# Optimization experiments

Measured on AMD Instinct MI355X. Metric: run time of the kernel, lower is better.

## Reference

```python
import jax, jax.numpy as jnp
import numpy as np

B, S, H = 4, 1024, 1024
NH, HD = 16, 64          # heads, head_dim (NH*HD == H)
E, K, I = 8, 2, 1024     # routed experts, top_k, expert intermediate
NSH = 2                  # shared experts -> shared intermediate = NSH*I
EPS = 1e-6


def setup_inputs() -> dict:
    key = jax.random.key(0)
    ks = jax.random.split(key, 12)
    init = lambda k, shape: (jax.random.normal(k, shape, jnp.float32) * 0.02)
    return {
        "hidden_states": jax.random.normal(ks[0], (B, S, H), jnp.float32),
        "conditioning": jax.random.normal(ks[1], (B, H), jnp.float32),
        "adaLN_W": init(ks[2], (H, 6 * H)),
        "ln1_scale": jnp.ones((H,), jnp.float32),
        "ln1_bias": jnp.zeros((H,), jnp.float32),
        "ln2_scale": jnp.ones((H,), jnp.float32),
        "ln2_bias": jnp.zeros((H,), jnp.float32),
        "Wq": init(ks[3], (H, H)),
        "Wk": init(ks[4], (H, H)),
        "Wv": init(ks[5], (H, H)),
        "Wo": init(ks[6], (H, H)),
        "gate_kernel": init(ks[7], (E, H)),
        "We1": init(ks[8], (E, H, I)),
        "We2": init(ks[9], (E, I, H)),
        "Ws1": init(ks[10], (H, NSH * I)),
        "Ws2": init(ks[11], (NSH * I, H)),
    }


def _layernorm(x, scale, bias):
    m = x.mean(-1, keepdims=True)
    v = x.var(-1, keepdims=True)
    return (x - m) * jax.lax.rsqrt(v + EPS) * scale + bias


def _modulate(x, shift, scale):
    # (1 + scale) * x + shift, broadcasting [B,H] conditioning over seq dim
    return x * (1.0 + scale[:, None, :]) + shift[:, None, :]


def _attention(x, Wq, Wk, Wv, Wo):
    b, s, h = x.shape
    q = (x @ Wq).reshape(b, s, NH, HD)
    k = (x @ Wk).reshape(b, s, NH, HD)
    v = (x @ Wv).reshape(b, s, NH, HD)
    scores = jnp.einsum("bqnd,bknd->bnqk", q, k) / np.sqrt(HD).astype(np.float32)
    probs = jax.nn.softmax(scores, axis=-1)
    out = jnp.einsum("bnqk,bknd->bqnd", probs, v).reshape(b, s, h)
    return out @ Wo


def reference(hidden_states, conditioning, adaLN_W, ln1_scale, ln1_bias,
              ln2_scale, ln2_bias, Wq, Wk, Wv, Wo, gate_kernel, We1, We2,
              Ws1, Ws2):
    # adaLN modulation: SiLU -> Linear(H, 6H) -> chunk 6
    mods = jax.nn.silu(conditioning) @ adaLN_W  # [B, 6H]
    (shift_msa, scale_msa, gate_msa,
     shift_mlp, scale_mlp, gate_mlp) = jnp.split(mods, 6, axis=-1)

    normed = _modulate(_layernorm(hidden_states, ln1_scale, ln1_bias),
                       shift_msa, scale_msa)
    attn_out = _attention(normed, Wq, Wk, Wv, Wo)
    h = hidden_states + gate_msa[:, None, :] * attn_out

    normed2 = _modulate(_layernorm(h, ln2_scale, ln2_bias),
                        shift_mlp, scale_mlp)

    # --- MoE gate (DeepSeek-V2 style, greedy top-k, softmax scoring) ---
    logits = jnp.einsum("bsh,eh->bse", normed2.astype(jnp.float32),
                        gate_kernel.astype(jnp.float32))
    scores = jax.nn.softmax(logits, axis=-1)           # [B,S,E]
    topk_w, topk_idx = jax.lax.top_k(scores, K)        # [B,S,K]
    topk_w = topk_w / (topk_w.sum(-1, keepdims=True) + 1e-20)  # norm_topk_prob

    # --- dense all-expert MLPs then top-k combine (as in DiTMLPMoE) ---
    eh = jax.nn.gelu(jnp.einsum("bsh,ehi->ebsi", normed2, We1))  # [E,B,S,I]
    eo = jnp.einsum("ebsi,eih->bseh", eh, We2)                   # [B,S,E,H]
    sel = jnp.take_along_axis(eo, topk_idx[..., None], axis=2)   # [B,S,K,H]
    y = (sel * topk_w[..., None].astype(sel.dtype)).sum(axis=2)  # [B,S,H]

    # shared experts (always active)
    y = y + jax.nn.gelu(normed2 @ Ws1) @ Ws2

    return h + gate_mlp[:, None, :] * y
```

## Files before the change

### kernel.cpp

```cpp
#include <hip/hip_runtime.h>

typedef __bf16 bf16x8 __attribute__((ext_vector_type(8)));
typedef __bf16 bf16x4 __attribute__((ext_vector_type(4)));
typedef float  f32x4  __attribute__((ext_vector_type(4)));

__device__ inline float wred_sum(float v){
  #pragma unroll
  for (int d = 1; d < 64; d <<= 1) v += __shfl_xor(v, d, 64);
  return v;
}

__device__ inline float gelu_t(float x){
  const float c0 = 0.7978845608028654f;
  float t = tanhf(c0 * (x + 0.044715f * x * x * x));
  return 0.5f * x * (1.0f + t);
}

__device__ __forceinline__ void gload_lds16(const __bf16* g, __bf16* l){
  __builtin_amdgcn_global_load_lds((const __attribute__((address_space(1))) void*)g,
                                   (__attribute__((address_space(3))) void*)l, 16, 0, 0);
}

__global__ __launch_bounds__(256)
void transpose_cvt(const float* __restrict__ in, __bf16* __restrict__ out, int R, int C){
  long mo = (long)blockIdx.z * R * C;
  in += mo; out += mo;
  __shared__ float t[32][33];
  int r0 = blockIdx.y * 32, c0 = blockIdx.x * 32;
  int tid = threadIdx.x;
  int tr = tid >> 3, tc = (tid & 7) * 4;
  float4 vv = *(const float4*)&in[(long)(r0 + tr) * C + c0 + tc];
  t[tr][tc + 0] = vv.x; t[tr][tc + 1] = vv.y; t[tr][tc + 2] = vv.z; t[tr][tc + 3] = vv.w;
  __syncthreads();
  int oc = tid >> 3, orr = (tid & 7) * 4;
  bf16x4 o4;
  #pragma unroll
  for (int i = 0; i < 4; i++) o4[i] = (__bf16)t[orr + i][oc];
  *(bf16x4*)&out[(long)(c0 + oc) * R + r0 + orr] = o4;
}

__global__ __launch_bounds__(256)
void adaln_k(const float* __restrict__ cond, const float* __restrict__ W, float* __restrict__ mods){
  int b = blockIdx.y, z = blockIdx.z;
  int col = (blockIdx.x * 256 + threadIdx.x) * 4;
  __shared__ float sc[256];
  int h2 = z * 256 + threadIdx.x;
  float x = cond[b * 1024 + h2];
  sc[threadIdx.x] = x / (1.f + expf(-x));
  __syncthreads();
  float a0 = 0.f, a1 = 0.f, a2 = 0.f, a3 = 0.f;
  #pragma unroll 4
  for (int i = 0; i < 256; i++){
    float s = sc[i];
    float4 wv = *(const float4*)&W[(long)(z * 256 + i) * 6144 + col];
    a0 += s * wv.x; a1 += s * wv.y; a2 += s * wv.z; a3 += s * wv.w;
  }
  atomicAdd(&mods[b * 6144 + col + 0], a0);
  atomicAdd(&mods[b * 6144 + col + 1], a1);
  atomicAdd(&mods[b * 6144 + col + 2], a2);
  atomicAdd(&mods[b * 6144 + col + 3], a3);
}

__global__ __launch_bounds__(256)
void ln_mod(const float* __restrict__ x, const float* __restrict__ sc, const float* __restrict__ bi,
            const float* __restrict__ mods, int shift_off, int scale_off, __bf16* __restrict__ out){
  int row = blockIdx.x, tid = threadIdx.x, b = row >> 10;
  float4 xv = *(const float4*)&x[(long)row * 1024 + tid * 4];
  float s  = xv.x + xv.y + xv.z + xv.w;
  float s2 = xv.x * xv.x + xv.y * xv.y + xv.z * xv.z + xv.w * xv.w;
  s = wred_sum(s); s2 = wred_sum(s2);
  __shared__ float ssum[4], ssum2[4];
  int w = tid >> 6;
  if ((tid & 63) == 0){ ssum[w] = s; ssum2[w] = s2; }
  __syncthreads();
  s = ssum[0] + ssum[1] + ssum[2] + ssum[3];
  s2 = ssum2[0] + ssum2[1] + ssum2[2] + ssum2[3];
  float mean = s * (1.f / 1024.f);
  float var  = s2 * (1.f / 1024.f) - mean * mean;
  float inv  = rsqrtf(var + 1e-6f);
  const float xa[4] = {xv.x, xv.y, xv.z, xv.w};
  #pragma unroll
  for (int i = 0; i < 4; i++){
    int c = tid * 4 + i;
    float nv = (xa[i] - mean) * inv * sc[c] + bi[c];
    nv = nv * (1.f + mods[b * 6144 + scale_off + c]) + mods[b * 6144 + shift_off + c];
    out[(long)row * 1024 + c] = (__bf16)nv;
  }
}

__global__ __launch_bounds__(256)
void gate_k(const float* __restrict__ h, const float* __restrict__ ln2s, const float* __restrict__ ln2b,
            const float* __restrict__ mods, const float* __restrict__ gw,
            int* __restrict__ eidx, float* __restrict__ wpair){
  __shared__ float gws[8192];
  int tid = threadIdx.x;
  #pragma unroll
  for (int i = 0; i < 8; i++){
    int idx = tid + i * 256;
    *(float4*)&gws[idx * 4] = *(const float4*)&gw[idx * 4];
  }
  __syncthreads();
  int wv = tid >> 6, lane = tid & 63;
  int tok = blockIdx.x * 4 + wv;
  int b = tok >> 10;
  float4 xv[4]; float s = 0.f, s2 = 0.f;
  #pragma unroll
  for (int ch = 0; ch < 4; ch++){
    float4 v = *(const float4*)&h[(long)tok * 1024 + ch * 256 + lane * 4];
    xv[ch] = v;
    s  += v.x + v.y + v.z + v.w;
    s2 += v.x * v.x + v.y * v.y + v.z * v.z + v.w * v.w;
  }
  s = wred_sum(s); s2 = wred_sum(s2);
  float mean = s * (1.f / 1024.f);
  float var  = s2 * (1.f / 1024.f) - mean * mean;
  float inv  = rsqrtf(var + 1e-6f);
  float lg[8];
  #pragma unroll
  for (int e = 0; e < 8; e++) lg[e] = 0.f;
  #pragma unroll
  for (int ch = 0; ch < 4; ch++){
    int c = ch * 256 + lane * 4;
    float4 s4  = *(const float4*)&ln2s[c];
    float4 b4  = *(const float4*)&ln2b[c];
    float4 sc4 = *(const float4*)&mods[b * 6144 + 4096 + c];
    float4 sh4 = *(const float4*)&mods[b * 6144 + 3072 + c];
    float n0 = ((xv[ch].x - mean) * inv * s4.x + b4.x) * (1.f + sc4.x) + sh4.x;
    float n1 = ((xv[ch].y - mean) * inv * s4.y + b4.y) * (1.f + sc4.y) + sh4.y;
    float n2 = ((xv[ch].z - mean) * inv * s4.z + b4.z) * (1.f + sc4.z) + sh4.z;
    float n3 = ((xv[ch].w - mean) * inv * s4.w + b4.w) * (1.f + sc4.w) + sh4.w;
    #pragma unroll
    for (int e = 0; e < 8; e++){
      float4 g4 = *(const float4*)&gws[e * 1024 + c];
      lg[e] += n0 * g4.x + n1 * g4.y + n2 * g4.z + n3 * g4.w;
    }
  }
  #pragma unroll
  for (int e = 0; e < 8; e++) lg[e] = wred_sum(lg[e]);
  if (lane == 0){
    float mx = lg[0];
    #pragma unroll
    for (int e = 1; e < 8; e++) mx = fmaxf(mx, lg[e]);
    float p[8], ss = 0.f;
    #pragma unroll
    for (int e = 0; e < 8; e++){ p[e] = expf(lg[e] - mx); ss += p[e]; }
    #pragma unroll
    for (int e = 0; e < 8; e++) p[e] /= ss;
    int i0 = 0; float b0 = p[0];
    #pragma unroll
    for (int e = 1; e < 8; e++) if (p[e] > b0){ b0 = p[e]; i0 = e; }
    int i1 = -1; float b1 = -1.f;
    #pragma unroll
    for (int e = 0; e < 8; e++) if (e != i0 && p[e] > b1){ b1 = p[e]; i1 = e; }
    float dn = b0 + b1 + 1e-20f;
    eidx[tok * 2]     = i0; wpair[tok * 2]     = b0 / dn;
    eidx[tok * 2 + 1] = i1; wpair[tok * 2 + 1] = b1 / dn;
  }
}

__global__ __launch_bounds__(256)
void build_k(const int* __restrict__ eidx, int* __restrict__ counts, int* __restrict__ lists){
  int e = blockIdx.x;
  int tid = threadIdx.x, wv = tid >> 6, lane = tid & 63;
  __shared__ int base;
  __shared__ int woff[4];
  if (tid == 0) base = 0;
  __syncthreads();
  for (int it = 0; it < 32; ++it){
    int i = it * 256 + tid;
    bool m = (eidx[i] == e);
    unsigned long long bal = __ballot(m);
    int prefix = __popcll(bal & ((1ull << lane) - 1ull));
    if (lane == 0) woff[wv] = __popcll(bal);
    __syncthreads();
    int off = base;
    #pragma unroll
    for (int k = 0; k < 4; k++) if (k < wv) off += woff[k];
    if (m) lists[e * 4096 + off + prefix] = i;
    __syncthreads();
    if (tid == 0) base += woff[0] + woff[1] + woff[2] + woff[3];
    __syncthreads();
  }
  if (tid == 0) counts[e] = base;
}

__global__ __launch_bounds__(256)
void attn_k(const __bf16* __restrict__ qkv, __bf16* __restrict__ og){
  int bh = blockIdx.y; int bb = bh >> 4, hn = bh & 15;
  int q0 = blockIdx.x * 128;
  long tokbase = (long)bb * 1024;
  int hd0 = hn * 64;
  int tid = threadIdx.x; int w = tid >> 6; int lane = tid & 63;

  __shared__ __bf16 Ks[64][76];
  __shared__ __bf16 Vt[64][76];
  __shared__ __bf16 Ps[4][32][76];

  const float QS = 0.125f * 1.44269504088896f;
  bf16x8 qf[2][2];
  #pragma unroll
  for (int sub = 0; sub < 2; sub++){
    long qrow = tokbase + q0 + sub * 64 + w * 16 + (lane & 15);
    qf[sub][0] = *(const bf16x8*)&qkv[qrow * 3072 + hd0 + (lane >> 4) * 8];
    qf[sub][1] = *(const bf16x8*)&qkv[qrow * 3072 + hd0 + 32 + (lane >> 4) * 8];
    #pragma unroll
    for (int i = 0; i < 8; i++){
      qf[sub][0][i] = (__bf16)((float)qf[sub][0][i] * QS);
      qf[sub][1][i] = (__bf16)((float)qf[sub][1][i] * QS);
    }
  }

  __bf16 one_b = (__bf16)1.0f;
  bf16x8 one8 = (bf16x8){one_b, one_b, one_b, one_b, one_b, one_b, one_b, one_b};

  float m_r[2][4];
  f32x4 oa[2][4];
  f32x4 lacc[2];
  #pragma unroll
  for (int sub = 0; sub < 2; sub++){
    lacc[sub] = (f32x4){0.f, 0.f, 0.f, 0.f};
    #pragma unroll
    for (int r = 0; r < 4; r++) m_r[sub][r] = -1e30f;
    #pragma unroll
    for (int hb = 0; hb < 4; hb++) oa[sub][hb] = (f32x4){0.f, 0.f, 0.f, 0.f};
  }

  int dcol = tid & 63, rblk = tid >> 6;
  for (int t = 0; t < 16; t++){
    long kvbase = tokbase + t * 64;
    #pragma unroll
    for (int p = 0; p < 2; p++){
      int r = (tid >> 3) + p * 32;
      int c = (tid & 7) * 8;
      *(bf16x8*)&Ks[r][c] = *(const bf16x8*)&qkv[(kvbase + r) * 3072 + 1024 + hd0 + c];
    }
    bf16x8 col0, col1;
    #pragma unroll
    for (int i = 0; i < 8; i++)
      col0[i] = qkv[(kvbase + rblk * 16 + i) * 3072 + 2048 + hd0 + dcol];
    #pragma unroll
    for (int i = 0; i < 8; i++)
      col1[i] = qkv[(kvbase + rblk * 16 + 8 + i) * 3072 + 2048 + hd0 + dcol];
    *(bf16x8*)&Vt[dcol][rblk * 16]     = col0;
    *(bf16x8*)&Vt[dcol][rblk * 16 + 8] = col1;
    __syncthreads();

    #pragma unroll
    for (int sub = 0; sub < 2; sub++){
      f32x4 sf[4];
      #pragma unroll
      for (int cb = 0; cb < 4; cb++){
        bf16x8 kf0 = *(const bf16x8*)&Ks[cb * 16 + (lane & 15)][(lane >> 4) * 8];
        bf16x8 kf1 = *(const bf16x8*)&Ks[cb * 16 + (lane & 15)][32 + (lane >> 4) * 8];
        f32x4 sacc = (f32x4){0.f, 0.f, 0.f, 0.f};
        sacc = __builtin_amdgcn_mfma_f32_16x16x32_bf16(qf[sub][0], kf0, sacc, 0, 0, 0);
        sacc = __builtin_amdgcn_mfma_f32_16x16x32_bf16(qf[sub][1], kf1, sacc, 0, 0, 0);
        sf[cb] = sacc;
      }
      float mxr[4]; float dmax = -1e30f;
      #pragma unroll
      for (int r = 0; r < 4; r++){
        float mx = fmaxf(fmaxf(sf[0][r], sf[1][r]), fmaxf(sf[2][r], sf[3][r]));
        #pragma unroll
        for (int d = 1; d < 16; d <<= 1) mx = fmaxf(mx, __shfl_xor(mx, d, 64));
        mxr[r] = mx;
        dmax = fmaxf(dmax, mx - m_r[sub][r]);
      }
      if (!__all(dmax <= 8.f)){
        #pragma unroll
        for (int r = 0; r < 4; r++){
          float mn = fmaxf(m_r[sub][r], mxr[r]);
          float fr = __builtin_amdgcn_exp2f(m_r[sub][r] - mn);
          m_r[sub][r] = mn;
          lacc[sub][r] *= fr;
          #pragma unroll
          for (int hb = 0; hb < 4; hb++) oa[sub][hb][r] *= fr;
        }
      }
      #pragma unroll
      for (int cb = 0; cb < 4; cb++)
        #pragma unroll
        for (int r = 0; r < 4; r++)
          Ps[w][sub * 16 + (lane >> 4) * 4 + r][cb * 16 + (lane & 15)] =
            (__bf16)__builtin_amdgcn_exp2f(sf[cb][r] - m_r[sub][r]);
    }
    bf16x8 pf[2][2];
    #pragma unroll
    for (int sub = 0; sub < 2; sub++){
      pf[sub][0] = *(const bf16x8*)&Ps[w][sub * 16 + (lane & 15)][(lane >> 4) * 8];
      pf[sub][1] = *(const bf16x8*)&Ps[w][sub * 16 + (lane & 15)][32 + (lane >> 4) * 8];
      lacc[sub] = __builtin_amdgcn_mfma_f32_16x16x32_bf16(pf[sub][0], one8, lacc[sub], 0, 0, 0);
      lacc[sub] = __builtin_amdgcn_mfma_f32_16x16x32_bf16(pf[sub][1], one8, lacc[sub], 0, 0, 0);
    }
    #pragma unroll
    for (int hb = 0; hb < 4; hb++){
      bf16x8 vf0 = *(const bf16x8*)&Vt[hb * 16 + (lane & 15)][(lane >> 4) * 8];
      bf16x8 vf1 = *(const bf16x8*)&Vt[hb * 16 + (lane & 15)][32 + (lane >> 4) * 8];
      #pragma unroll
      for (int sub = 0; sub < 2; sub++){
        oa[sub][hb] = __builtin_amdgcn_mfma_f32_16x16x32_bf16(pf[sub][0], vf0, oa[sub][hb], 0, 0, 0);
        oa[sub][hb] = __builtin_amdgcn_mfma_f32_16x16x32_bf16(pf[sub][1], vf1, oa[sub][hb], 0, 0, 0);
      }
    }
    __syncthreads();
  }
  #pragma unroll
  for (int sub = 0; sub < 2; sub++)
    #pragma unroll
    for (int hb = 0; hb < 4; hb++)
      #pragma unroll
      for (int r = 0; r < 4; r++){
        long row = tokbase + q0 + sub * 64 + w * 16 + (lane >> 4) * 4 + r;
        float val = oa[sub][hb][r] / lacc[sub][r];
        og[row * 1024 + hd0 + hb * 16 + (lane & 15)] = (__bf16)val;
      }
}

template<int EPI, int GMODE>
__global__ __launch_bounds__(256)
void gemm_k(const __bf16* __restrict__ A, int lda,
            const __bf16* __restrict__ Bt, int K, long bstride,
            const int* __restrict__ lists, const int* __restrict__ counts,
            __bf16* __restrict__ outb, int ldo,
            float* __restrict__ outf,
            const float* __restrict__ resid,
            const float* __restrict__ mods, int mod_off,
            const float* __restrict__ wpair){
  int e = blockIdx.z;
  int cnt = 1 << 30;
  const int* list = nullptr;
  if (GMODE){
    cnt = counts[e];
    if ((int)blockIdx.y * 128 >= cnt) return;
    list = lists + e * 4096;
    Bt += (long)e * bstride;
  }
  int row0 = blockIdx.y * 128;
  int n0 = blockIdx.x * 128;
  int tid = threadIdx.x;
  int lane = tid & 63, w = tid >> 6;
  int wr = (w >> 1) * 64, wc = (w & 1) * 64;

  __shared__ __bf16 As[128 * 64];
  __shared__ __bf16 Bs[128 * 64];

  f32x4 acc[4][4];
  #pragma unroll
  for (int m = 0; m < 4; m++)
    #pragma unroll
    for (int n = 0; n < 4; n++) acc[m][n] = (f32x4){0.f, 0.f, 0.f, 0.f};

  long aoff[4]; const __bf16* bptr[4];
  #pragma unroll
  for (int j = 0; j < 4; j++){
    int r = w * 32 + j * 8 + (lane >> 3);
    int scb = (lane & 7) ^ (r & 7);
    int gr = row0 + r;
    int srcr;
    if (GMODE == 0) srcr = gr;
    else if (gr < cnt){ int pv = list[gr]; srcr = (GMODE == 1) ? (pv >> 1) : pv; }
    else { int pv = list[0]; srcr = (GMODE == 1) ? (pv >> 1) : pv; }
    aoff[j] = (long)srcr * lda + scb * 8;
    bptr[j] = Bt + (long)(n0 + r) * K + scb * 8;
  }
  const int nk = K / 64;
  for (int kt = 0; kt < nk; ++kt){
    int k0 = kt * 64;
    #pragma unroll
    for (int j = 0; j < 4; j++){
      gload_lds16(A + aoff[j] + k0, &As[(w * 32 + j * 8) * 64]);
      gload_lds16(bptr[j] + k0,     &Bs[(w * 32 + j * 8) * 64]);
    }
    __syncthreads();
    #pragma unroll
    for (int ks = 0; ks < 2; ++ks){
      bf16x8 af[4], bfr[4];
      #pragma unroll
      for (int m = 0; m < 4; m++){
        int r = wr + m * 16 + (lane & 15);
        int blk = (ks * 4 + (lane >> 4)) ^ (r & 7);
        af[m] = *(const bf16x8*)&As[r * 64 + blk * 8];
      }
      #pragma unroll
      for (int n = 0; n < 4; n++){
        int r = wc + n * 16 + (lane & 15);
        int blk = (ks * 4 + (lane >> 4)) ^ (r & 7);
        bfr[n] = *(const bf16x8*)&Bs[r * 64 + blk * 8];
      }
      #pragma unroll
      for (int m = 0; m < 4; m++)
        #pragma unroll
        for (int n = 0; n < 4; n++)
          acc[m][n] = __builtin_amdgcn_mfma_f32_16x16x32_bf16(af[m], bfr[n], acc[m][n], 0, 0, 0);
    }
    __syncthreads();
  }
  #pragma unroll
  for (int m = 0; m < 4; m++){
    #pragma unroll
    for (int r = 0; r < 4; r++){
      int rl = wr + m * 16 + (lane >> 4) * 4 + r;
      int grow = row0 + rl;
      if (GMODE && grow >= cnt) continue;
      #pragma unroll
      for (int n = 0; n < 4; n++){
        int col = n0 + wc + n * 16 + (lane & 15);
        float v = acc[m][n][r];
        if (EPI == 0){
          outb[(long)grow * ldo + col] = (__bf16)v;
        } else if (EPI == 1){
          int dst = (GMODE == 1) ? list[grow] : grow;
          outb[(long)dst * ldo + col] = (__bf16)gelu_t(v);
        } else if (EPI == 2){
          int b = grow >> 10;
          outf[(long)grow * 1024 + col] = resid[(long)grow * 1024 + col] + mods[b * 6144 + mod_off + col] * v;
        } else if (EPI == 3){
          outf[(long)grow * 1024 + col] = v;
        } else if (EPI == 4){
          int pv = list[grow];
          atomicAdd(&outf[(long)(pv >> 1) * 1024 + col], wpair[pv] * v);
        }
      }
    }
  }
}

__global__ __launch_bounds__(256)
void final_k(const float* __restrict__ h, const float* __restrict__ y,
             const float* __restrict__ mods, float* __restrict__ out){
  int i = blockIdx.x * 256 + threadIdx.x;
  long base = (long)i * 4;
  int row = (int)(base >> 10); int b = row >> 10; int c = (int)(base & 1023);
  float4 hv = *(const float4*)&h[base];
  float4 yv = *(const float4*)&y[base];
  const float* g = &mods[b * 6144 + 5120 + c];
  float4 o;
  o.x = hv.x + g[0] * yv.x;
  o.y = hv.y + g[1] * yv.y;
  o.z = hv.z + g[2] * yv.z;
  o.w = hv.w + g[3] * yv.w;
  *(float4*)&out[base] = o;
}

extern "C" void kernel_launch(void* const* d_in, const int* in_sizes, int n_in,
                              void* d_out, int out_size, void* d_ws, size_t ws_size,
                              hipStream_t stream){
  const float* hidden = (const float*)d_in[0];
  const float* cond   = (const float*)d_in[1];
  const float* adaW   = (const float*)d_in[2];
  const float* ln1s   = (const float*)d_in[3];
  const float* ln1b   = (const float*)d_in[4];
  const float* ln2s   = (const float*)d_in[5];
  const float* ln2b   = (const float*)d_in[6];
  const float* Wq     = (const float*)d_in[7];
  const float* Wk     = (const float*)d_in[8];
  const float* Wv     = (const float*)d_in[9];
  const float* Wo     = (const float*)d_in[10];
  const float* gatek  = (const float*)d_in[11];
  const float* We1    = (const float*)d_in[12];
  const float* We2    = (const float*)d_in[13];
  const float* Ws1    = (const float*)d_in[14];
  const float* Ws2    = (const float*)d_in[15];
  float* out = (float*)d_out;

  const size_t MB = 1024 * 1024;
  char* W = (char*)d_ws;
  size_t off = 0;
  auto take = [&](size_t b) -> void* {
    void* p = W + off;
    off += (b + 255) & ~((size_t)255);
    return p;
  };
  float*  mods   = (float*) take(4 * 6144 * sizeof(float));
  __bf16* qkvT   = (__bf16*)take(6 * MB);
  __bf16* WoT    = (__bf16*)take(2 * MB);
  __bf16* Ws1T   = (__bf16*)take(4 * MB);
  __bf16* Ws2T   = (__bf16*)take(4 * MB);
  __bf16* We1T   = (__bf16*)take(16 * MB);
  __bf16* We2T   = (__bf16*)take(16 * MB);
  __bf16* n1     = (__bf16*)take(8 * MB);
  __bf16* ab     = (__bf16*)take(8 * MB);
  __bf16* qkv    = (__bf16*)take(24 * MB);
  float*  hb     = (float*) take(16 * MB);
  __bf16* n2     = (__bf16*)take(8 * MB);
  float*  yb     = (float*) take(16 * MB);
  int*    counts = (int*)   take(256);
  int*    lists  = (int*)   take(8 * 4096 * 4);
  float*  wpair  = (float*) take(8192 * 4);
  int*    eidx   = (int*)   take(8192 * 4);
  __bf16* EH = n1;
  __bf16* SH = qkv;

  dim3 blk(256);

  hipMemsetAsync(mods, 0, 4 * 6144 * sizeof(float), stream);

  transpose_cvt<<<dim3(32, 32, 1), blk, 0, stream>>>(Wq,  qkvT,              1024, 1024);
  transpose_cvt<<<dim3(32, 32, 1), blk, 0, stream>>>(Wk,  qkvT + 1024*1024,  1024, 1024);
  transpose_cvt<<<dim3(32, 32, 1), blk, 0, stream>>>(Wv,  qkvT + 2048*1024,  1024, 1024);
  transpose_cvt<<<dim3(32, 32, 1), blk, 0, stream>>>(Wo,  WoT,  1024, 1024);
  transpose_cvt<<<dim3(64, 32, 1), blk, 0, stream>>>(Ws1, Ws1T, 1024, 2048);
  transpose_cvt<<<dim3(32, 64, 1), blk, 0, stream>>>(Ws2, Ws2T, 2048, 1024);
  transpose_cvt<<<dim3(32, 32, 8), blk, 0, stream>>>(We1, We1T, 1024, 1024);
  transpose_cvt<<<dim3(32, 32, 8), blk, 0, stream>>>(We2, We2T, 1024, 1024);

  adaln_k<<<dim3(6, 4, 4), blk, 0, stream>>>(cond, adaW, mods);

  ln_mod<<<4096, blk, 0, stream>>>(hidden, ln1s, ln1b, mods, 0, 1024, n1);

  gemm_k<0, 0><<<dim3(24, 32, 1), blk, 0, stream>>>(n1, 1024, qkvT, 1024, 0, nullptr, nullptr, qkv, 3072, nullptr, nullptr, nullptr, 0, nullptr);

  attn_k<<<dim3(8, 64, 1), blk, 0, stream>>>(qkv, ab);

  gemm_k<2, 0><<<dim3(8, 32, 1), blk, 0, stream>>>(ab, 1024, WoT, 1024, 0, nullptr, nullptr, nullptr, 0, hb, hidden, mods, 2048, nullptr);

  ln_mod<<<4096, blk, 0, stream>>>(hb, ln2s, ln2b, mods, 3072, 4096, n2);

  gate_k<<<1024, blk, 0, stream>>>(hb, ln2s, ln2b, mods, gatek, eidx, wpair);
  build_k<<<8, blk, 0, stream>>>(eidx, counts, lists);

  gemm_k<1, 0><<<dim3(16, 32, 1), blk, 0, stream>>>(n2, 1024, Ws1T, 1024, 0, nullptr, nullptr, SH, 2048, nullptr, nullptr, nullptr, 0, nullptr);
  gemm_k<3, 0><<<dim3(8, 32, 1), blk, 0, stream>>>(SH, 2048, Ws2T, 2048, 0, nullptr, nullptr, nullptr, 0, yb, nullptr, nullptr, 0, nullptr);

  gemm_k<1, 1><<<dim3(8, 32, 8), blk, 0, stream>>>(n2, 1024, We1T, 1024, 1048576, lists, counts, EH, 1024, nullptr, nullptr, nullptr, 0, nullptr);
  gemm_k<4, 2><<<dim3(8, 32, 8), blk, 0, stream>>>(EH, 1024, We2T, 1024, 1048576, lists, counts, nullptr, 0, yb, nullptr, nullptr, 0, wpair);

  final_k<<<4096, blk, 0, stream>>>(hb, yb, mods, out);

  (void)in_sizes; (void)n_in; (void)out_size; (void)ws_size;
}
```

Baseline: 561.7 us.

## Fuse transposes, LN2 into gate, final combine into shared GEMM; double-buffer GEMM LDS

All weight transposes now run in one launch. adaLN is restructured so each block handles all four batches and reuses each weight load. The second layernorm-modulate is folded into the gate kernel, and the final residual/gate combine is folded into the shared-expert down-projection epilogue, which removes two launches and a full activation pass. The routed-expert accumulator is zeroed by the same memset. The GEMM main loop gains double-buffered LDS with prefetch of the next K tile, doubling shared memory use and possibly lowering occupancy. Attention blocks are also remapped so neighbouring blocks share KV.

New measurement: 560.9 us. About the same (-0.1%).

```diff
diff --git a/kernel.cpp b/kernel.cpp
--- a/kernel.cpp
+++ b/kernel.cpp
@@ -22,43 +22,58 @@
 }
 
 __global__ __launch_bounds__(256)
-void transpose_cvt(const float* __restrict__ in, __bf16* __restrict__ out, int R, int C){
-  long mo = (long)blockIdx.z * R * C;
-  in += mo; out += mo;
+void transpose_all(const float* __restrict__ Wq, const float* __restrict__ Wk,
+                   const float* __restrict__ Wv, const float* __restrict__ Wo,
+                   const float* __restrict__ Ws1, const float* __restrict__ Ws2,
+                   const float* __restrict__ We1, const float* __restrict__ We2,
+                   __bf16* __restrict__ qkvT, __bf16* __restrict__ WoT,
+                   __bf16* __restrict__ Ws1T, __bf16* __restrict__ Ws2T,
+                   __bf16* __restrict__ We1T, __bf16* __restrict__ We2T){
+  int z = blockIdx.z;
+  const float* src; long ss; __bf16* dst; long ds;
+  const long M1 = 1024 * 1024;
+  if (z < 3)      { src = (z == 0 ? Wq : z == 1 ? Wk : Wv); ss = 1024; dst = qkvT + (long)z * M1; ds = 1024; }
+  else if (z == 3){ src = Wo; ss = 1024; dst = WoT; ds = 1024; }
+  else if (z < 6) { int ch = z - 4; src = Ws1 + ch * 1024; ss = 2048; dst = Ws1T + (long)ch * M1; ds = 1024; }
+  else if (z < 8) { int rh = z - 6; src = Ws2 + (long)rh * M1; ss = 1024; dst = Ws2T + rh * 1024; ds = 2048; }
+  else if (z < 16){ int e = z - 8;  src = We1 + (long)e * M1; ss = 1024; dst = We1T + (long)e * M1; ds = 1024; }
+  else            { int e = z - 16; src = We2 + (long)e * M1; ss = 1024; dst = We2T + (long)e * M1; ds = 1024; }
   __shared__ float t[32][33];
   int r0 = blockIdx.y * 32, c0 = blockIdx.x * 32;
   int tid = threadIdx.x;
   int tr = tid >> 3, tc = (tid & 7) * 4;
-  float4 vv = *(const float4*)&in[(long)(r0 + tr) * C + c0 + tc];
+  float4 vv = *(const float4*)&src[(long)(r0 + tr) * ss + c0 + tc];
   t[tr][tc + 0] = vv.x; t[tr][tc + 1] = vv.y; t[tr][tc + 2] = vv.z; t[tr][tc + 3] = vv.w;
   __syncthreads();
   int oc = tid >> 3, orr = (tid & 7) * 4;
   bf16x4 o4;
   #pragma unroll
   for (int i = 0; i < 4; i++) o4[i] = (__bf16)t[orr + i][oc];
-  *(bf16x4*)&out[(long)(c0 + oc) * R + r0 + orr] = o4;
+  *(bf16x4*)&dst[(long)(c0 + oc) * ds + r0 + orr] = o4;
 }
 
 __global__ __launch_bounds__(256)
 void adaln_k(const float* __restrict__ cond, const float* __restrict__ W, float* __restrict__ mods){
-  int b = blockIdx.y, z = blockIdx.z;
-  int col = (blockIdx.x * 256 + threadIdx.x) * 4;
-  __shared__ float sc[256];
-  int h2 = z * 256 + threadIdx.x;
-  float x = cond[b * 1024 + h2];
-  sc[threadIdx.x] = x / (1.f + expf(-x));
+  int col = blockIdx.x * 256 + threadIdx.x;
+  int kc  = blockIdx.y;
+  __shared__ float sc[4][256];
+  for (int i = threadIdx.x; i < 1024; i += 256){
+    int b = i >> 8, r = i & 255;
+    float x = cond[b * 1024 + kc * 256 + r];
+    sc[b][r] = x / (1.f + expf(-x));
+  }
   __syncthreads();
   float a0 = 0.f, a1 = 0.f, a2 = 0.f, a3 = 0.f;
   #pragma unroll 4
   for (int i = 0; i < 256; i++){
-    float s = sc[i];
-    float4 wv = *(const float4*)&W[(long)(z * 256 + i) * 6144 + col];
-    a0 += s * wv.x; a1 += s * wv.y; a2 += s * wv.z; a3 += s * wv.w;
-  }
-  atomicAdd(&mods[b * 6144 + col + 0], a0);
-  atomicAdd(&mods[b * 6144 + col + 1], a1);
-  atomicAdd(&mods[b * 6144 + col + 2], a2);
-  atomicAdd(&mods[b * 6144 + col + 3], a3);
+    float wv = W[(long)(kc * 256 + i) * 6144 + col];
+    a0 += sc[0][i] * wv; a1 += sc[1][i] * wv;
+    a2 += sc[2][i] * wv; a3 += sc[3][i] * wv;
+  }
+  atomicAdd(&mods[0 * 6144 + col], a0);
+  atomicAdd(&mods[1 * 6144 + col], a1);
+  atomicAdd(&mods[2 * 6144 + col], a2);
+  atomicAdd(&mods[3 * 6144 + col], a3);
 }
 
 __global__ __launch_bounds__(256)
@@ -91,7 +106,7 @@
 __global__ __launch_bounds__(256)
 void gate_k(const float* __restrict__ h, const float* __restrict__ ln2s, const float* __restrict__ ln2b,
             const float* __restrict__ mods, const float* __restrict__ gw,
-            int* __restrict__ eidx, float* __restrict__ wpair){
+            int* __restrict__ eidx, float* __restrict__ wpair, __bf16* __restrict__ n2o){
   __shared__ float gws[8192];
   int tid = threadIdx.x;
   #pragma unroll
@@ -125,14 +140,15 @@
     float4 b4  = *(const float4*)&ln2b[c];
     float4 sc4 = *(const float4*)&mods[b * 6144 + 4096 + c];
     float4 sh4 = *(const float4*)&mods[b * 6144 + 3072 + c];
-    float n0 = ((xv[ch].x - mean) * inv * s4.x + b4.x) * (1.f + sc4.x) + sh4.x;
-    float n1 = ((xv[ch].y - mean) * inv * s4.y + b4.y) * (1.f + sc4.y) + sh4.y;
-    float n2 = ((xv[ch].z - mean) * inv * s4.z + b4.z) * (1.f + sc4.z) + sh4.z;
-    float n3 = ((xv[ch].w - mean) * inv * s4.w + b4.w) * (1.f + sc4.w) + sh4.w;
+    float v0 = ((xv[ch].x - mean) * inv * s4.x + b4.x) * (1.f + sc4.x) + sh4.x;
+    float v1 = ((xv[ch].y - mean) * inv * s4.y + b4.y) * (1.f + sc4.y) + sh4.y;
+    float v2 = ((xv[ch].z - mean) * inv * s4.z + b4.z) * (1.f + sc4.z) + sh4.z;
+    float v3 = ((xv[ch].w - mean) * inv * s4.w + b4.w) * (1.f + sc4.w) + sh4.w;
+    *(bf16x4*)&n2o[(long)tok * 1024 + c] = (bf16x4){(__bf16)v0, (__bf16)v1, (__bf16)v2, (__bf16)v3};
     #pragma unroll
     for (int e = 0; e < 8; e++){
       float4 g4 = *(const float4*)&gws[e * 1024 + c];
-      lg[e] += n0 * g4.x + n1 * g4.y + n2 * g4.z + n3 * g4.w;
+      lg[e] += v0 * g4.x + v1 * g4.y + v2 * g4.z + v3 * g4.w;
     }
   }
   #pragma unroll
@@ -186,8 +202,11 @@
 
 __global__ __launch_bounds__(256)
 void attn_k(const __bf16* __restrict__ qkv, __bf16* __restrict__ og){
-  int bh = blockIdx.y; int bb = bh >> 4, hn = bh & 15;
-  int q0 = blockIdx.x * 128;
+  int p = blockIdx.x + blockIdx.y * 8;
+  int qblk = (p >> 3) & 7;
+  int bh   = (p & 7) + ((p >> 6) << 3);
+  int bb = bh >> 4, hn = bh & 15;
+  int q0 = qblk * 128;
   long tokbase = (long)bb * 1024;
   int hd0 = hn * 64;
   int tid = threadIdx.x; int w = tid >> 6; int lane = tid & 63;
@@ -229,8 +248,8 @@
   for (int t = 0; t < 16; t++){
     long kvbase = tokbase + t * 64;
     #pragma unroll
-    for (int p = 0; p < 2; p++){
-      int r = (tid >> 3) + p * 32;
+    for (int pp = 0; pp < 2; pp++){
+      int r = (tid >> 3) + pp * 32;
       int c = (tid & 7) * 8;
       *(bf16x8*)&Ks[r][c] = *(const bf16x8*)&qkv[(kvbase + r) * 3072 + 1024 + hd0 + c];
     }
@@ -325,7 +344,8 @@
             float* __restrict__ outf,
             const float* __restrict__ resid,
             const float* __restrict__ mods, int mod_off,
-            const float* __restrict__ wpair){
+            const float* __restrict__ wpair,
+            const float* __restrict__ addin){
   int e = blockIdx.z;
   int cnt = 1 << 30;
   const int* list = nullptr;
@@ -341,8 +361,8 @@
   int lane = tid & 63, w = tid >> 6;
   int wr = (w >> 1) * 64, wc = (w & 1) * 64;
 
-  __shared__ __bf16 As[128 * 64];
-  __shared__ __bf16 Bs[128 * 64];
+  __shared__ __bf16 As[2 * 128 * 64];
+  __shared__ __bf16 Bs[2 * 128 * 64];
 
   f32x4 acc[4][4];
   #pragma unroll
@@ -364,14 +384,23 @@
     bptr[j] = Bt + (long)(n0 + r) * K + scb * 8;
   }
   const int nk = K / 64;
+  #pragma unroll
+  for (int j = 0; j < 4; j++){
+    gload_lds16(A + aoff[j], &As[(w * 32 + j * 8) * 64]);
+    gload_lds16(bptr[j],     &Bs[(w * 32 + j * 8) * 64]);
+  }
+  __syncthreads();
+  int cur = 0;
   for (int kt = 0; kt < nk; ++kt){
-    int k0 = kt * 64;
-    #pragma unroll
-    for (int j = 0; j < 4; j++){
-      gload_lds16(A + aoff[j] + k0, &As[(w * 32 + j * 8) * 64]);
-      gload_lds16(bptr[j] + k0,     &Bs[(w * 32 + j * 8) * 64]);
-    }
-    __syncthreads();
+    int nxt = cur ^ 1;
+    if (kt + 1 < nk){
+      int k0 = (kt + 1) * 64;
+      #pragma unroll
+      for (int j = 0; j < 4; j++){
+        gload_lds16(A + aoff[j] + k0, &As[nxt * 8192 + (w * 32 + j * 8) * 64]);
+        gload_lds16(bptr[j] + k0,     &Bs[nxt * 8192 + (w * 32 + j * 8) * 64]);
+      }
+    }
     #pragma unroll
     for (int ks = 0; ks < 2; ++ks){
       bf16x8 af[4], bfr[4];
@@ -379,13 +408,13 @@
       for (int m = 0; m < 4; m++){
         int r = wr + m * 16 + (lane & 15);
         int blk = (ks * 4 + (lane >> 4)) ^ (r & 7);
-        af[m] = *(const bf16x8*)&As[r * 64 + blk * 8];
+        af[m] = *(const bf16x8*)&As[cur * 8192 + r * 64 + blk * 8];
       }
       #pragma unroll
       for (int n = 0; n < 4; n++){
         int r = wc + n * 16 + (lane & 15);
         int blk = (ks * 4 + (lane >> 4)) ^ (r & 7);
-        bfr[n] = *(const bf16x8*)&Bs[r * 64 + blk * 8];
+        bfr[n] = *(const bf16x8*)&Bs[cur * 8192 + r * 64 + blk * 8];
       }
       #pragma unroll
       for (int m = 0; m < 4; m++)
@@ -394,6 +423,7 @@
           acc[m][n] = __builtin_amdgcn_mfma_f32_16x16x32_bf16(af[m], bfr[n], acc[m][n], 0, 0, 0);
     }
     __syncthreads();
+    cur = nxt;
   }
   #pragma unroll
   for (int m = 0; m < 4; m++){
@@ -414,32 +444,17 @@
         } else if (EPI == 2){
           int b = grow >> 10;
           outf[(long)grow * 1024 + col] = resid[(long)grow * 1024 + col] + mods[b * 6144 + mod_off + col] * v;
-        } else if (EPI == 3){
-          outf[(long)grow * 1024 + col] = v;
         } else if (EPI == 4){
           int pv = list[grow];
           atomicAdd(&outf[(long)(pv >> 1) * 1024 + col], wpair[pv] * v);
+        } else if (EPI == 5){
+          int b = grow >> 10;
+          outf[(long)grow * 1024 + col] = resid[(long)grow * 1024 + col]
+              + mods[b * 6144 + mod_off + col] * (v + addin[(long)grow * 1024 + col]);
         }
       }
     }
   }
-}
-
-__global__ __launch_bounds__(256)
-void final_k(const float* __restrict__ h, const float* __restrict__ y,
-             const float* __restrict__ mods, float* __restrict__ out){
-  int i = blockIdx.x * 256 + threadIdx.x;
-  long base = (long)i * 4;
-  int row = (int)(base >> 10); int b = row >> 10; int c = (int)(base & 1023);
-  float4 hv = *(const float4*)&h[base];
-  float4 yv = *(const float4*)&y[base];
-  const float* g = &mods[b * 6144 + 5120 + c];
-  float4 o;
-  o.x = hv.x + g[0] * yv.x;
-  o.y = hv.y + g[1] * yv.y;
-  o.z = hv.z + g[2] * yv.z;
-  o.w = hv.w + g[3] * yv.w;
-  *(float4*)&out[base] = o;
 }
 
 extern "C" void kernel_launch(void* const* d_in, const int* in_sizes, int n_in,
@@ -472,6 +487,7 @@
     return p;
   };
   float*  mods   = (float*) take(4 * 6144 * sizeof(float));
+  float*  yb     = (float*) take(16 * MB);
   __bf16* qkvT   = (__bf16*)take(6 * MB);
   __bf16* WoT    = (__bf16*)take(2 * MB);
   __bf16* Ws1T   = (__bf16*)take(4 * MB);
@@ -483,7 +499,6 @@
   __bf16* qkv    = (__bf16*)take(24 * MB);
   float*  hb     = (float*) take(16 * MB);
   __bf16* n2     = (__bf16*)take(8 * MB);
-  float*  yb     = (float*) take(16 * MB);
   int*    counts = (int*)   take(256);
   int*    lists  = (int*)   take(8 * 4096 * 4);
   float*  wpair  = (float*) take(8192 * 4);
@@ -493,39 +508,29 @@
 
   dim3 blk(256);
 
-  hipMemsetAsync(mods, 0, 4 * 6144 * sizeof(float), stream);
-
-  transpose_cvt<<<dim3(32, 32, 1), blk, 0, stream>>>(Wq,  qkvT,              1024, 1024);
-  transpose_cvt<<<dim3(32, 32, 1), blk, 0, stream>>>(Wk,  qkvT + 1024*1024,  1024, 1024);
-  transpose_cvt<<<dim3(32, 32, 1), blk, 0, stream>>>(Wv,  qkvT + 2048*1024,  1024, 1024);
-  transpose_cvt<<<dim3(32, 32, 1), blk, 0, stream>>>(Wo,  WoT,  1024, 1024);
-  transpose_cvt<<<dim3(64, 32, 1), blk, 0, stream>>>(Ws1, Ws1T, 1024, 2048);
-  transpose_cvt<<<dim3(32, 64, 1), blk, 0, stream>>>(Ws2, Ws2T, 2048, 1024);
-  transpose_cvt<<<dim3(32, 32, 8), blk, 0, stream>>>(We1, We1T, 1024, 1024);
-  transpose_cvt<<<dim3(32, 32, 8), blk, 0, stream>>>(We2, We2T, 1024, 1024);
-
-  adaln_k<<<dim3(6, 4, 4), blk, 0, stream>>>(cond, adaW, mods);
+  hipMemsetAsync(mods, 0, 4 * 6144 * sizeof(float) + 16 * MB, stream);
+
+  transpose_all<<<dim3(32, 32, 24), blk, 0, stream>>>(Wq, Wk, Wv, Wo, Ws1, Ws2, We1, We2,
+                                                      qkvT, WoT, Ws1T, Ws2T, We1T, We2T);
+
+  adaln_k<<<dim3(24, 4), blk, 0, stream>>>(cond, adaW, mods);
 
   ln_mod<<<4096, blk, 0, stream>>>(hidden, ln1s, ln1b, mods, 0, 1024, n1);
 
-  gemm_k<0, 0><<<dim3(24, 32, 1), blk, 0, stream>>>(n1, 1024, qkvT, 1024, 0, nullptr, nullptr, qkv, 3072, nullptr, nullptr, nullptr, 0, nullptr);
+  gemm_k<0, 0><<<dim3(24, 32, 1), blk, 0, stream>>>(n1, 1024, qkvT, 1024, 0, nullptr, nullptr, qkv, 3072, nullptr, nullptr, nullptr, 0, nullptr, nullptr);
 
   attn_k<<<dim3(8, 64, 1), blk, 0, stream>>>(qkv, ab);
 
-  gemm_k<2, 0><<<dim3(8, 32, 1), blk, 0, stream>>>(ab, 1024, WoT, 1024, 0, nullptr, nullptr, nullptr, 0, hb, hidden, mods, 2048, nullptr);
-
-  ln_mod<<<4096, blk, 0, stream>>>(hb, ln2s, ln2b, mods, 3072, 4096, n2);
-
-  gate_k<<<1024, blk, 0, stream>>>(hb, ln2s, ln2b, mods, gatek, eidx, wpair);
+  gemm_k<2, 0><<<dim3(8, 32, 1), blk, 0, stream>>>(ab, 1024, WoT, 1024, 0, nullptr, nullptr, nullptr, 0, hb, hidden, mods, 2048, nullptr, nullptr);
+
+  gate_k<<<1024, blk, 0, stream>>>(hb, ln2s, ln2b, mods, gatek, eidx, wpair, n2);
   build_k<<<8, blk, 0, stream>>>(eidx, counts, lists);
 
-  gemm_k<1, 0><<<dim3(16, 32, 1), blk, 0, stream>>>(n2, 1024, Ws1T, 1024, 0, nullptr, nullptr, SH, 2048, nullptr, nullptr, nullptr, 0, nullptr);
-  gemm_k<3, 0><<<dim3(8, 32, 1), blk, 0, stream>>>(SH, 2048, Ws2T, 2048, 0, nullptr, nullptr, nullptr, 0, yb, nullptr, nullptr, 0, nullptr);
-
-  gemm_k<1, 1><<<dim3(8, 32, 8), blk, 0, stream>>>(n2, 1024, We1T, 1024, 1048576, lists, counts, EH, 1024, nullptr, nullptr, nullptr, 0, nullptr);
-  gemm_k<4, 2><<<dim3(8, 32, 8), blk, 0, stream>>>(EH, 1024, We2T, 1024, 1048576, lists, counts, nullptr, 0, yb, nullptr, nullptr, 0, wpair);
-
-  final_k<<<4096, blk, 0, stream>>>(hb, yb, mods, out);
+  gemm_k<1, 1><<<dim3(8, 32, 8), blk, 0, stream>>>(n2, 1024, We1T, 1024, 1048576, lists, counts, EH, 1024, nullptr, nullptr, nullptr, 0, nullptr, nullptr);
+  gemm_k<4, 2><<<dim3(8, 32, 8), blk, 0, stream>>>(EH, 1024, We2T, 1024, 1048576, lists, counts, nullptr, 0, yb, nullptr, nullptr, 0, wpair, nullptr);
+
+  gemm_k<1, 0><<<dim3(16, 32, 1), blk, 0, stream>>>(n2, 1024, Ws1T, 1024, 0, nullptr, nullptr, SH, 2048, nullptr, nullptr, nullptr, 0, nullptr, nullptr);
+  gemm_k<5, 0><<<dim3(8, 32, 1), blk, 0, stream>>>(SH, 2048, Ws2T, 2048, 0, nullptr, nullptr, nullptr, 0, out, hb, mods, 5120, nullptr, yb);
 
   (void)in_sizes; (void)n_in; (void)out_size; (void)ws_size;
 }
```
